# Kernel optimization log

Measured on AMD Instinct MI355X. Metric: run time of the kernel, lower is better.

The kernel has to match this reference:

```python
import jax, jax.numpy as jnp
import numpy as np

BOUND = 10.0
EPS = 1e-06
MIN_SCALE = 1e-4


def _params_to_spline(raw_w, raw_h, raw_s, bound):
    # Standard Durkan et al. rational-quadratic spline parameterization.
    # raw_w/raw_h: (1, D, K); raw_s: (1, D, K+1)
    two_b = 2.0 * bound
    widths = jax.nn.softmax(raw_w[0], axis=-1) * two_b      # (D, K)
    heights = jax.nn.softmax(raw_h[0], axis=-1) * two_b     # (D, K)
    zero = jnp.zeros(widths.shape[:-1] + (1,), widths.dtype)
    xk = -bound + jnp.concatenate([zero, jnp.cumsum(widths, axis=-1)], axis=-1)   # (D, K+1)
    yk = -bound + jnp.concatenate([zero, jnp.cumsum(heights, axis=-1)], axis=-1)  # (D, K+1)
    slopes = jax.nn.softplus(raw_s[0])                       # (D, K+1)
    return xk, yk, widths, heights, slopes


def _rqs_forward(z, xk, yk, widths, heights, slopes, bound):
    # z: (B, D); per-dim knots xk/yk: (D, K+1); widths/heights: (D, K); slopes: (D, K+1)
    B, D = z.shape
    K = widths.shape[-1]
    zc = jnp.clip(z, -bound, bound)
    # per-dim binary search over knot positions
    idx = jax.vmap(lambda knots, col: jnp.searchsorted(knots, col, side='right'),
                   in_axes=(0, 1), out_axes=1)(xk, zc) - 1
    idx = jnp.clip(idx, 0, K - 1)                            # (B, D)
    di = jnp.arange(D)[None, :]
    xk_sel = xk[di, idx]
    w_sel = widths[di, idx]
    yk_sel = yk[di, idx]
    h_sel = heights[di, idx]
    d0 = slopes[di, idx]
    d1 = slopes[di, idx + 1]
    theta = (zc - xk_sel) / w_sel
    s = h_sel / w_sel
    t1m = theta * (1.0 - theta)
    den = s + (d0 + d1 - 2.0 * s) * t1m
    y_in = yk_sel + h_sel * (s * theta * theta + d0 * t1m) / den
    inside = (z > -bound) & (z < bound)
    return jnp.where(inside, y_in, z)


def setup_inputs() -> dict:
    key = jax.random.key(0)
    ks = jax.random.split(key, 7)
    B, D, K = 8192, 1024, 64
    return {
        'u': jax.random.uniform(ks[0], (B, D), dtype=jnp.float32),
        'tau': jax.random.normal(ks[1], (B, 1), dtype=jnp.float32),
        'log_scale': jax.random.normal(ks[2], (D,), dtype=jnp.float32) * 0.1,
        'bias': jax.random.normal(ks[3], (D,), dtype=jnp.float32) * 0.1,
        'raw_w': jax.random.normal(ks[4], (1, D, K), dtype=jnp.float32) * 0.5,
        'raw_h': jax.random.normal(ks[5], (1, D, K), dtype=jnp.float32) * 0.5,
        'raw_s': jax.random.normal(ks[6], (1, D, K + 1), dtype=jnp.float32) * 0.5,
    }


def reference(u, tau, log_scale, bias, raw_w, raw_h, raw_s):
    # logit input transform
    u_safe = jnp.clip(u, EPS, 1.0 - EPS)
    z = jnp.log(u_safe) - jnp.log1p(-u_safe)
    xk, yk, widths, heights, slopes = _params_to_spline(raw_w, raw_h, raw_s, BOUND)
    z = _rqs_forward(z, xk, yk, widths, heights, slopes, BOUND)
    scale = jax.nn.softplus(log_scale) + MIN_SCALE
    q = z * scale[None, :] + bias[None, :]
    return tau * q  # tau (B,1) broadcasts to (B,D)
```

## Files before the change

### kernel.cpp

```cpp
#include <hip/hip_runtime.h>
#include <math.h>

#define BOUNDF 10.0f
#define EPSF 1e-6f
#define MIN_SCALEF 1e-4f
#define DD 1024
#define KK 64
#define KP1 65

#define TD 16
#define NCELL 256
#define TR 256
#define ITER (TR / 64)

__device__ __forceinline__ float softplus_f(float x) {
    return fmaxf(x, 0.0f) + __logf(1.0f + __expf(-fabsf(x)));
}

__global__ __launch_bounds__(256, 5) void rqs_fused(
    const float* __restrict__ u, const float* __restrict__ tau,
    const float* __restrict__ log_scale, const float* __restrict__ bias,
    const float* __restrict__ raw_w, const float* __restrict__ raw_h,
    const float* __restrict__ raw_s, float* __restrict__ out)
{
    __shared__ float4 livt[TD * KK];
    __shared__ float  lxk[TD * KP1];
    __shared__ float  lsl[TD * KP1];
    __shared__ unsigned char lgr[TD * NCELL];

    const int bx = blockIdx.x;
    const int dchunk = bx & (DD / TD - 1);
    const int rchunk = bx >> 6;
    const int d0 = dchunk * TD;
    const int r0 = rchunk * TR;
    const int t = threadIdx.x;
    const int wv = t >> 6;
    const int lane = t & 63;

    for (int jd = 0; jd < 4; ++jd) {
        const int dl = wv * 4 + jd;
        const int d = d0 + dl;
        float ew = __expf(raw_w[d * KK + lane]);
        float eh = __expf(raw_h[d * KK + lane]);
        float sw = ew, sh = eh;
#pragma unroll
        for (int off = 1; off < 64; off <<= 1) {
            sw += __shfl_xor(sw, off, 64);
            sh += __shfl_xor(sh, off, 64);
        }
        float wk = ew * ((2.0f * BOUNDF) / sw);
        float hk = eh * ((2.0f * BOUNDF) / sh);
        float cw = wk, ch = hk;
#pragma unroll
        for (int off = 1; off < 64; off <<= 1) {
            float aw = __shfl_up(cw, off, 64);
            float ah = __shfl_up(ch, off, 64);
            if (lane >= off) { cw += aw; ch += ah; }
        }
        float cwp = __shfl_up(cw, 1, 64); if (lane == 0) cwp = 0.0f;
        float chp = __shfl_up(ch, 1, 64); if (lane == 0) chp = 0.0f;
        float X  = -BOUNDF + cwp;
        float Yv = -BOUNDF + chp;
        float Xn = (lane == 63) ? BOUNDF : (-BOUNDF + cw);
        float Yn = (lane == 63) ? BOUNDF : (-BOUNDF + ch);
        float invw = 1.0f / (Xn - X);
        livt[dl * KK + lane] = make_float4(X, Yv, invw, Yn - Yv);
        lxk[dl * KP1 + lane] = X;
        lsl[dl * KP1 + lane] = softplus_f(raw_s[d * KP1 + lane]);
        if (lane == 63) {
            lxk[dl * KP1 + 64] = BOUNDF;
            lsl[dl * KP1 + 64] = softplus_f(raw_s[d * KP1 + 64]);
        }
        int c0 = (int)ceilf(cwp * (NCELL / (2.0f * BOUNDF)));
        int c1 = (lane == 63) ? NCELL
                              : (int)ceilf(cw * (NCELL / (2.0f * BOUNDF)));
        c1 = min(c1, NCELL);
        for (int c = c0; c < c1; ++c) lgr[dl * NCELL + c] = (unsigned char)lane;
    }
    __syncthreads();

    const int g4 = (t & 3) * 4;
    const int rl = t >> 2;
    const int dg = d0 + g4;

    float sc[4], bi[4];
#pragma unroll
    for (int j = 0; j < 4; ++j) {
        sc[j] = softplus_f(log_scale[dg + j]) + MIN_SCALEF;
        bi[j] = bias[dg + j];
    }

    int b = r0 + rl;
    float4 uu = *(const float4*)(u + (size_t)b * DD + dg);
    float tb = tau[b];

#pragma unroll 1
    for (int it = 0; it < ITER; ++it) {
        const float4 ucur = uu;
        const float tcur = tb;
        const int bcur = b;
        if (it + 1 < ITER) {
            b += 64;
            uu = *(const float4*)(u + (size_t)b * DD + dg);
            tb = tau[b];
        }
        float ua[4] = {ucur.x, ucur.y, ucur.z, ucur.w};
        float res[4];
#pragma unroll
        for (int j = 0; j < 4; ++j) {
            float uv = fminf(fmaxf(ua[j], EPSF), 1.0f - EPSF);
            float z = __logf(uv * __builtin_amdgcn_rcpf(1.0f - uv));
            float zc = fminf(fmaxf(z, -BOUNDF), 9.9999990f);
            const int bxk = (g4 + j) * KP1;
            int cell = (int)fmaf(zc, NCELL / (2.0f * BOUNDF), 0.5f * NCELL);
            int lo = (int)lgr[(g4 + j) * NCELL + cell];
            float nx = lxk[bxk + lo + 1];
            bool adv = (nx <= zc);
            while (__any(adv)) {
                lo += adv;
                nx = lxk[bxk + lo + 1];
                adv = adv && (nx <= zc);
            }
            float4 iv = livt[(g4 + j) * KK + lo];
            float dd0 = lsl[bxk + lo];
            float dd1 = lsl[bxk + lo + 1];
            float th  = (zc - iv.x) * iv.z;
            float s   = iv.w * iv.z;
            float t1m = th * (1.0f - th);
            float den = fmaf(fmaf(-2.0f, s, dd0 + dd1), t1m, s);
            float num = iv.w * fmaf(s * th, th, dd0 * t1m);
            float y = fmaf(num, __builtin_amdgcn_rcpf(den), iv.y);
            y = (fabsf(z) < BOUNDF) ? y : z;
            res[j] = tcur * fmaf(y, sc[j], bi[j]);
        }
        *(float4*)(out + (size_t)bcur * DD + dg) =
            make_float4(res[0], res[1], res[2], res[3]);
    }
}

extern "C" void kernel_launch(void* const* d_in, const int* in_sizes, int n_in,
                              void* d_out, int out_size, void* d_ws, size_t ws_size,
                              hipStream_t stream)
{
    const float* u         = (const float*)d_in[0];
    const float* tau       = (const float*)d_in[1];
    const float* log_scale = (const float*)d_in[2];
    const float* bias      = (const float*)d_in[3];
    const float* raw_w     = (const float*)d_in[4];
    const float* raw_h     = (const float*)d_in[5];
    const float* raw_s     = (const float*)d_in[6];
    float* out = (float*)d_out;

    const int B = in_sizes[0] / DD;
    rqs_fused<<<(DD / TD) * (B / TR), 256, 0, stream>>>(
        u, tau, log_scale, bias, raw_w, raw_h, raw_s, out);
}
```

Measured before the change: 115.6 us.

## Split spline table build into a precompute kernel and load tables in main kernel

Moves the per-dimension softmax, cumsum, softplus and cell-grid construction into a separate small kernel that writes tables to workspace. The main kernel then only copies those tables into shared memory instead of recomputing them in every block, and reads knot x positions from the float4 table instead of a separate array. It also doubles the rows per block and lowers the occupancy hint. The cost is a second launch and a global-memory round trip for the tables.

```diff
diff --git a/kernel.cpp b/kernel.cpp
--- a/kernel.cpp
+++ b/kernel.cpp
@@ -10,21 +10,69 @@
 
 #define TD 16
 #define NCELL 256
-#define TR 256
+#define TR 512
 #define ITER (TR / 64)
+#define CPB (NCELL / (2.0f * BOUNDF))
 
 __device__ __forceinline__ float softplus_f(float x) {
     return fmaxf(x, 0.0f) + __logf(1.0f + __expf(-fabsf(x)));
 }
 
-__global__ __launch_bounds__(256, 5) void rqs_fused(
+__global__ __launch_bounds__(64) void rqs_precompute(
+    const float* __restrict__ raw_w, const float* __restrict__ raw_h,
+    const float* __restrict__ raw_s, const float* __restrict__ log_scale,
+    float4* __restrict__ ivt_g, float* __restrict__ sl_g,
+    unsigned char* __restrict__ grid_g, float* __restrict__ scale_g)
+{
+    const int d = blockIdx.x;
+    const int k = threadIdx.x;
+
+    float ew = __expf(raw_w[d * KK + k]);
+    float eh = __expf(raw_h[d * KK + k]);
+    float sw = ew, sh = eh;
+#pragma unroll
+    for (int off = 1; off < 64; off <<= 1) {
+        sw += __shfl_xor(sw, off, 64);
+        sh += __shfl_xor(sh, off, 64);
+    }
+    float wk = ew * ((2.0f * BOUNDF) / sw);
+    float hk = eh * ((2.0f * BOUNDF) / sh);
+    float cw = wk, ch = hk;
+#pragma unroll
+    for (int off = 1; off < 64; off <<= 1) {
+        float aw = __shfl_up(cw, off, 64);
+        float ah = __shfl_up(ch, off, 64);
+        if (k >= off) { cw += aw; ch += ah; }
+    }
+    float cwp = __shfl_up(cw, 1, 64); if (k == 0) cwp = 0.0f;
+    float chp = __shfl_up(ch, 1, 64); if (k == 0) chp = 0.0f;
+    float X  = -BOUNDF + cwp;
+    float Yv = -BOUNDF + chp;
+    float Xn = (k == 63) ? BOUNDF : (-BOUNDF + cw);
+    float Yn = (k == 63) ? BOUNDF : (-BOUNDF + ch);
+    ivt_g[d * KP1 + k] = make_float4(X, Yv, 1.0f / (Xn - X), Yn - Yv);
+    sl_g[d * KP1 + k] = softplus_f(raw_s[d * KP1 + k]);
+    if (k == 63) {
+        ivt_g[d * KP1 + 64] = make_float4(BOUNDF, BOUNDF, 0.0f, 0.0f);
+    }
+    if (k == 0) {
+        sl_g[d * KP1 + 64] = softplus_f(raw_s[d * KP1 + KK]);
+        scale_g[d] = softplus_f(log_scale[d]) + MIN_SCALEF;
+    }
+    int c0 = (int)ceilf(cwp * CPB);
+    int c1 = (k == 63) ? NCELL : (int)ceilf(cw * CPB);
+    c1 = min(c1, NCELL);
+    for (int c = c0; c < c1; ++c) grid_g[d * NCELL + c] = (unsigned char)k;
+}
+
+__global__ __launch_bounds__(256, 4) void rqs_main(
     const float* __restrict__ u, const float* __restrict__ tau,
-    const float* __restrict__ log_scale, const float* __restrict__ bias,
-    const float* __restrict__ raw_w, const float* __restrict__ raw_h,
-    const float* __restrict__ raw_s, float* __restrict__ out)
+    const float* __restrict__ bias,
+    const float4* __restrict__ ivt_g, const float* __restrict__ sl_g,
+    const unsigned char* __restrict__ grid_g, const float* __restrict__ scale_g,
+    float* __restrict__ out)
 {
-    __shared__ float4 livt[TD * KK];
-    __shared__ float  lxk[TD * KP1];
+    __shared__ float4 livt[TD * KP1];
     __shared__ float  lsl[TD * KP1];
     __shared__ unsigned char lgr[TD * NCELL];
 
@@ -34,48 +82,15 @@
     const int d0 = dchunk * TD;
     const int r0 = rchunk * TR;
     const int t = threadIdx.x;
-    const int wv = t >> 6;
-    const int lane = t & 63;
 
-    for (int jd = 0; jd < 4; ++jd) {
-        const int dl = wv * 4 + jd;
-        const int d = d0 + dl;
-        float ew = __expf(raw_w[d * KK + lane]);
-        float eh = __expf(raw_h[d * KK + lane]);
-        float sw = ew, sh = eh;
-#pragma unroll
-        for (int off = 1; off < 64; off <<= 1) {
-            sw += __shfl_xor(sw, off, 64);
-            sh += __shfl_xor(sh, off, 64);
-        }
-        float wk = ew * ((2.0f * BOUNDF) / sw);
-        float hk = eh * ((2.0f * BOUNDF) / sh);
-        float cw = wk, ch = hk;
-#pragma unroll
-        for (int off = 1; off < 64; off <<= 1) {
-            float aw = __shfl_up(cw, off, 64);
-            float ah = __shfl_up(ch, off, 64);
-            if (lane >= off) { cw += aw; ch += ah; }
-        }
-        float cwp = __shfl_up(cw, 1, 64); if (lane == 0) cwp = 0.0f;
-        float chp = __shfl_up(ch, 1, 64); if (lane == 0) chp = 0.0f;
-        float X  = -BOUNDF + cwp;
-        float Yv = -BOUNDF + chp;
-        float Xn = (lane == 63) ? BOUNDF : (-BOUNDF + cw);
-        float Yn = (lane == 63) ? BOUNDF : (-BOUNDF + ch);
-        float invw = 1.0f / (Xn - X);
-        livt[dl * KK + lane] = make_float4(X, Yv, invw, Yn - Yv);
-        lxk[dl * KP1 + lane] = X;
-        lsl[dl * KP1 + lane] = softplus_f(raw_s[d * KP1 + lane]);
-        if (lane == 63) {
-            lxk[dl * KP1 + 64] = BOUNDF;
-            lsl[dl * KP1 + 64] = softplus_f(raw_s[d * KP1 + 64]);
-        }
-        int c0 = (int)ceilf(cwp * (NCELL / (2.0f * BOUNDF)));
-        int c1 = (lane == 63) ? NCELL
-                              : (int)ceilf(cw * (NCELL / (2.0f * BOUNDF)));
-        c1 = min(c1, NCELL);
-        for (int c = c0; c < c1; ++c) lgr[dl * NCELL + c] = (unsigned char)lane;
+    for (int i = t; i < TD * KP1; i += 256) {
+        livt[i] = ivt_g[d0 * KP1 + i];
+        lsl[i]  = sl_g[d0 * KP1 + i];
+    }
+    {
+        const unsigned int* gsrc = (const unsigned int*)(grid_g + d0 * NCELL);
+        unsigned int* gdst = (unsigned int*)lgr;
+        for (int i = t; i < TD * NCELL / 4; i += 256) gdst[i] = gsrc[i];
     }
     __syncthreads();
 
@@ -86,7 +101,7 @@
     float sc[4], bi[4];
 #pragma unroll
     for (int j = 0; j < 4; ++j) {
-        sc[j] = softplus_f(log_scale[dg + j]) + MIN_SCALEF;
+        sc[j] = scale_g[dg + j];
         bi[j] = bias[dg + j];
     }
 
@@ -111,19 +126,19 @@
             float uv = fminf(fmaxf(ua[j], EPSF), 1.0f - EPSF);
             float z = __logf(uv * __builtin_amdgcn_rcpf(1.0f - uv));
             float zc = fminf(fmaxf(z, -BOUNDF), 9.9999990f);
-            const int bxk = (g4 + j) * KP1;
-            int cell = (int)fmaf(zc, NCELL / (2.0f * BOUNDF), 0.5f * NCELL);
+            const int ib = (g4 + j) * KP1;
+            int cell = (int)fmaf(zc, CPB, 0.5f * NCELL);
             int lo = (int)lgr[(g4 + j) * NCELL + cell];
-            float nx = lxk[bxk + lo + 1];
+            float nx = livt[ib + lo + 1].x;
             bool adv = (nx <= zc);
             while (__any(adv)) {
                 lo += adv;
-                nx = lxk[bxk + lo + 1];
+                nx = livt[ib + lo + 1].x;
                 adv = adv && (nx <= zc);
             }
-            float4 iv = livt[(g4 + j) * KK + lo];
-            float dd0 = lsl[bxk + lo];
-            float dd1 = lsl[bxk + lo + 1];
+            float4 iv = livt[ib + lo];
+            float dd0 = lsl[ib + lo];
+            float dd1 = lsl[ib + lo + 1];
             float th  = (zc - iv.x) * iv.z;
             float s   = iv.w * iv.z;
             float t1m = th * (1.0f - th);
@@ -151,7 +166,16 @@
     const float* raw_s     = (const float*)d_in[6];
     float* out = (float*)d_out;
 
+    float* ws = (float*)d_ws;
+    float4* ivt = (float4*)ws;
+    float* sl = ws + (size_t)DD * KP1 * 4;
+    unsigned char* grid = (unsigned char*)(sl + DD * KP1);
+    float* scale = (float*)(grid + (size_t)DD * NCELL);
+
     const int B = in_sizes[0] / DD;
-    rqs_fused<<<(DD / TD) * (B / TR), 256, 0, stream>>>(
-        u, tau, log_scale, bias, raw_w, raw_h, raw_s, out);
+
+    rqs_precompute<<<DD, 64, 0, stream>>>(raw_w, raw_h, raw_s, log_scale,
+                                          ivt, sl, grid, scale);
+    rqs_main<<<(DD / TD) * (B / TR), 256, 0, stream>>>(
+        u, tau, bias, ivt, sl, grid, scale, out);
 }
```

Result: faster. 109.7 us (-5.1%).
